# Performance work log

Measured on AMD Instinct MI355X. Metric: run time of the kernel, lower is better.

## Reference

```python
import jax, jax.numpy as jnp
import numpy as np

DIM = 768
HEADS = 12
HEAD_DIM = DIM // HEADS
HIDDEN = 4 * DIM
LS_INIT = 1e-5
EPS = 1e-5


def layernorm(x, g, b):
    mu = jnp.mean(x, axis=-1, keepdims=True)
    var = jnp.mean(jnp.square(x - mu), axis=-1, keepdims=True)
    return (x - mu) * jax.lax.rsqrt(var + EPS) * g + b


def setup_inputs() -> dict:
    key = jax.random.key(0)
    ks = jax.random.split(key, 8)
    s = lambda fan_in: 1.0 / np.sqrt(fan_in)
    return {
        "x": jax.random.normal(ks[0], (8, 1024, DIM), dtype=jnp.float32),
        "ln1_g": jnp.ones((DIM,), jnp.float32),
        "ln1_b": jnp.zeros((DIM,), jnp.float32),
        "w_qkv": jax.random.uniform(ks[1], (3 * DIM, DIM), jnp.float32, -s(DIM), s(DIM)),
        "w_proj": jax.random.uniform(ks[2], (DIM, DIM), jnp.float32, -s(DIM), s(DIM)),
        "b_proj": jnp.zeros((DIM,), jnp.float32),
        "ls1_g": jnp.full((DIM,), LS_INIT, jnp.float32),
        "ln2_g": jnp.ones((DIM,), jnp.float32),
        "ln2_b": jnp.zeros((DIM,), jnp.float32),
        "w_fc1": jax.random.uniform(ks[3], (HIDDEN, DIM), jnp.float32, -s(DIM), s(DIM)),
        "b_fc1": jnp.zeros((HIDDEN,), jnp.float32),
        "w_fc2": jax.random.uniform(ks[4], (DIM, HIDDEN), jnp.float32, -s(HIDDEN), s(HIDDEN)),
        "b_fc2": jnp.zeros((DIM,), jnp.float32),
        "ls2_g": jnp.full((DIM,), LS_INIT, jnp.float32),
    }


def reference(x, ln1_g, ln1_b, w_qkv, w_proj, b_proj, ls1_g,
              ln2_g, ln2_b, w_fc1, b_fc1, w_fc2, b_fc2, ls2_g):
    B, N, C = x.shape
    # --- attention branch ---
    h = layernorm(x, ln1_g, ln1_b)
    qkv = h @ w_qkv.T  # [B,N,3C]
    qkv = qkv.reshape(B, N, 3, HEADS, HEAD_DIM)
    q, k, v = qkv[:, :, 0], qkv[:, :, 1], qkv[:, :, 2]  # [B,N,H,D]
    scale = 1.0 / np.sqrt(HEAD_DIM)
    attn = jnp.einsum("bqhd,bkhd->bhqk", q, k) * scale
    attn = jax.nn.softmax(attn, axis=-1)
    o = jnp.einsum("bhqk,bkhd->bqhd", attn, v).reshape(B, N, C)
    o = o @ w_proj.T + b_proj
    x = x + ls1_g * o
    # --- MLP branch ---
    h = layernorm(x, ln2_g, ln2_b)
    h = jax.nn.gelu(h @ w_fc1.T + b_fc1, approximate=False)
    h = h @ w_fc2.T + b_fc2
    x = x + ls2_g * h
    return x
```

## Files before the change

### kernel.cpp

```cpp
#include <hip/hip_runtime.h>
#include <cstdint>
#include <cstddef>

typedef __bf16 bf16x8 __attribute__((ext_vector_type(8)));
typedef float f32x4 __attribute__((ext_vector_type(4)));
typedef int i32x4 __attribute__((ext_vector_type(4)));
typedef int i32x8 __attribute__((ext_vector_type(8)));

__device__ __forceinline__ void gload16(const void* g, void* l) {
  __builtin_amdgcn_global_load_lds((const __attribute__((address_space(1))) void*)g,
                                   (__attribute__((address_space(3))) void*)l, 16, 0, 0);
}

__device__ __forceinline__ float exp2_fast(float x) {
  float r;
  asm("v_exp_f32 %0, %1" : "=v"(r) : "v"(x));
  return r;
}
__device__ __forceinline__ float rcp_fast(float x) {
  float r;
  asm("v_rcp_f32 %0, %1" : "=v"(r) : "v"(x));
  return r;
}

__device__ __forceinline__ unsigned int f32_to_fp4(float x) {
  const float a = fabsf(x);
  unsigned int c = a < 0.25f ? 0u : a < 0.75f ? 1u : a < 1.25f ? 2u : a < 1.75f ? 3u
                 : a < 2.5f  ? 4u : a < 3.5f  ? 5u : a < 5.0f  ? 6u : 7u;
  return c | ((__float_as_uint(x) >> 28) & 8u);
}
__device__ __forceinline__ unsigned char pack_fp4x2(float lo, float hi) {
  return (unsigned char)(f32_to_fp4(lo) | (f32_to_fp4(hi) << 4));
}

template<int N> __device__ __forceinline__ void wait_vm() {
  if constexpr (N == 0)       asm volatile("s_waitcnt vmcnt(0)" ::: "memory");
  else if constexpr (N == 3)  asm volatile("s_waitcnt vmcnt(3)" ::: "memory");
  else if constexpr (N == 4)  asm volatile("s_waitcnt vmcnt(4)" ::: "memory");
}

#define S_BARRIER() __builtin_amdgcn_s_barrier()
#define WAIT_LGKM() asm volatile("s_waitcnt lgkmcnt(0)" ::: "memory")

__global__ __launch_bounds__(256) void ln_kernel(const float* __restrict__ x,
    const float* __restrict__ g, const float* __restrict__ b,
    unsigned char* __restrict__ out)
{
  __shared__ float red[8];
  const int row = blockIdx.x, t = threadIdx.x;
  const float* xr = x + (size_t)row * 768;
  float v0 = xr[t], v1 = xr[t + 256], v2 = xr[t + 512];
  float s = v0 + v1 + v2;
  float q = v0 * v0 + v1 * v1 + v2 * v2;
  #pragma unroll
  for (int off = 32; off > 0; off >>= 1) {
    s += __shfl_xor(s, off, 64);
    q += __shfl_xor(q, off, 64);
  }
  const int w = t >> 6;
  if ((t & 63) == 0) { red[w] = s; red[4 + w] = q; }
  __syncthreads();
  s = red[0] + red[1] + red[2] + red[3];
  q = red[4] + red[5] + red[6] + red[7];
  const float mu = s * (1.0f / 768.0f);
  const float var = q * (1.0f / 768.0f) - mu * mu;
  const float rstd = rsqrtf(var + 1e-5f);
  unsigned char* orow = out + (size_t)row * 384;
  for (int p = t; p < 384; p += 256) {
    const int c = 2 * p;
    const float y0 = (xr[c]     - mu) * rstd * g[c]     + b[c];
    const float y1 = (xr[c + 1] - mu) * rstd * g[c + 1] + b[c + 1];
    orow[p] = pack_fp4x2(y0, y1);
  }
}

__global__ __launch_bounds__(256) void cast4_kernel(
    const float* __restrict__ i0, const float* __restrict__ i1,
    const float* __restrict__ i2, const float* __restrict__ i3,
    unsigned char* __restrict__ o0, unsigned char* __restrict__ o1,
    unsigned char* __restrict__ o2, unsigned char* __restrict__ o3)
{
  const int n0 = 2304 * 768 / 4, n1 = 768 * 768 / 4;
  const int n2 = 3072 * 768 / 4, n3 = 768 * 3072 / 4;
  const int total = n0 + n1 + n2 + n3;
  for (int i = blockIdx.x * 256 + threadIdx.x; i < total; i += gridDim.x * 256) {
    const float* in; unsigned char* out; int j = i; float ws = 128.0f;
    if (j < n0) { in = i0; out = o0; }
    else if ((j -= n0) < n1) { in = i1; out = o1; }
    else if ((j -= n1) < n2) { in = i2; out = o2; }
    else { j -= n2; in = i3; out = o3; ws = 256.0f; }
    float4 v = ((const float4*)in)[j];
    const unsigned char b0 = pack_fp4x2(v.x * ws, v.y * ws);
    const unsigned char b1 = pack_fp4x2(v.z * ws, v.w * ws);
    ((unsigned short*)out)[j] = (unsigned short)(b0 | (b1 << 8));
  }
}

template<int MODE>
__global__ __launch_bounds__(256) void gemm_kernel(
    const unsigned char* __restrict__ A, const unsigned char* __restrict__ W, int K,
    unsigned int scaleB,
    const float* __restrict__ bias, const float* __restrict__ resid,
    const float* __restrict__ ls, float* __restrict__ outf,
    unsigned char* __restrict__ outb,
    __bf16* __restrict__ qo, __bf16* __restrict__ ko, __bf16* __restrict__ vo)
{
  constexpr int FM = 4, FN = 2;
  __shared__ unsigned char As[2 * 128 * 64];
  __shared__ unsigned char Bs[2 * 64 * 64];

  const int nx = gridDim.x;
  const int nwg = nx * gridDim.y;
  const int orig = blockIdx.x + nx * blockIdx.y;
  const int nid = (orig & 7) * (nwg >> 3) + (orig >> 3);
  const int bx = nid % nx, by = nid / nx;

  const int t = threadIdx.x;
  const int lane = t & 63;
  const int w = t >> 6;
  const int wm = w >> 1, wn = w & 1;
  const int m0 = by * 128, n0 = bx * 64;
  const int rl = lane & 15, gs = lane >> 4;
  const int Kb2 = K >> 1;

  f32x4 acc[FM][FN];
  #pragma unroll
  for (int i = 0; i < FM; ++i)
    #pragma unroll
    for (int j = 0; j < FN; ++j) acc[i][j] = { 0.f, 0.f, 0.f, 0.f };

  const unsigned char* Asrc[2];
  const unsigned char* Bsrc1;
  #pragma unroll
  for (int i = 0; i < 2; ++i) {
    const int g = i * 256 + t, row = g >> 2, gc = g & 3;
    Asrc[i] = A + (size_t)(m0 + row) * Kb2 + ((gc ^ (row & 3)) << 4);
  }
  {
    const int row = t >> 2, gc = t & 3;
    Bsrc1 = W + (size_t)(n0 + row) * Kb2 + ((gc ^ (row & 3)) << 4);
  }

  auto stage = [&](int kt, int buf) {
    const int k0 = kt << 6;
    #pragma unroll
    for (int i = 0; i < 2; ++i)
      gload16(Asrc[i] + k0, As + buf * 8192 + (i * 256 + t) * 16);
    gload16(Bsrc1 + k0, Bs + buf * 4096 + t * 16);
  };

  auto ld16 = [&](const unsigned char* rowbase, int sw) -> i32x8 {
    const i32x4 v = *(const i32x4*)(rowbase + ((gs ^ sw) << 4));
    i32x8 r;
    r[0] = v[0]; r[1] = v[1]; r[2] = v[2]; r[3] = v[3];
    r[4] = 0; r[5] = 0; r[6] = 0; r[7] = 0;
    return r;
  };

  const int nk = K >> 7;
  stage(0, 0);

  #pragma unroll 2
  for (int kt = 0; kt < nk; ++kt) {
    const int cur = kt & 1;
    if (kt + 1 < nk) { stage(kt + 1, cur ^ 1); wait_vm<3>(); }
    else             { wait_vm<0>(); }
    S_BARRIER();

    const unsigned char* Ac = As + cur * 8192;
    const unsigned char* Bc = Bs + cur * 4096;
    i32x8 af[FM], bfr[FN];
    #pragma unroll
    for (int fm = 0; fm < FM; ++fm) {
      const int row = wm * 64 + fm * 16 + rl;
      af[fm] = ld16(Ac + row * 64, row & 3);
    }
    #pragma unroll
    for (int fn = 0; fn < FN; ++fn) {
      const int row = wn * 32 + fn * 16 + rl;
      bfr[fn] = ld16(Bc + row * 64, row & 3);
    }
    #pragma unroll
    for (int fm = 0; fm < FM; ++fm)
      #pragma unroll
      for (int fn = 0; fn < FN; ++fn)
        acc[fm][fn] = __builtin_amdgcn_mfma_scale_f32_16x16x128_f8f6f4(
            af[fm], bfr[fn], acc[fm][fn],
            4, 4,
            0, 0x7F7F7F7F,
            0, (int)scaleB);

    S_BARRIER();
  }

  #pragma unroll
  for (int fm = 0; fm < FM; ++fm) {
    const int rbase = m0 + wm * 64 + fm * 16 + gs * 4;
    #pragma unroll
    for (int fn = 0; fn < FN; ++fn) {
      const int c = n0 + wn * 32 + fn * 16 + rl;
      #pragma unroll
      for (int b = 0; b < 4; ++b) {
        const int r = rbase + b;
        const float val = acc[fm][fn][b];
        if constexpr (MODE == 0) {
          const int sec = c / 768;
          const int cc = c - sec * 768;
          const int hh = cc >> 6, d = cc & 63;
          const int batch = r >> 10, n = r & 1023;
          const size_t bh = (size_t)(batch * 12 + hh);
          if (sec == 0)      qo[(bh * 1024 + n) * 64 + d] = (__bf16)(val * 0.1803368801111204f);
          else if (sec == 1) ko[(bh * 1024 + n) * 64 + d] = (__bf16)val;
          else               vo[(bh * 64 + d) * 1024 + n] = (__bf16)val;
        } else if constexpr (MODE == 1) {
          const size_t idx = (size_t)r * 768 + c;
          outf[idx] = resid[idx] + ls[c] * (val + bias[c]);
        } else if constexpr (MODE == 2) {
          const float h = val + bias[c];
          const float z = h * (1.0f + 0.044715f * h * h);
          const float e = exp2_fast(2.3021181f * z);
          const float gl = h - h * rcp_fast(1.0f + e);
          const float gp = __shfl_xor(gl, 1, 64);
          if ((lane & 1) == 0)
            outb[(size_t)r * 1536 + (c >> 1)] = pack_fp4x2(gl, gp);
        } else {
          const size_t idx = (size_t)r * 768 + c;
          outf[idx] = resid[idx] + ls[c] * (val + bias[c]);
        }
      }
    }
  }
}

__global__ __launch_bounds__(256, 3) void attn_kernel(
    const __bf16* __restrict__ Q, const __bf16* __restrict__ Kb,
    const __bf16* __restrict__ Vt, unsigned char* __restrict__ Ob)
{
  __shared__ __bf16 Ks[2][64 * 64];
  __shared__ __bf16 Vs[2][64 * 64];
  __shared__ __bf16 P_lds[4][32 * 72];

  const int nid = blockIdx.x;
  const int b7 = nid & 7, rest = nid >> 3;
  const int qt = rest & 7;
  const int bh = b7 + ((rest >> 3) << 3);

  const int t = threadIdx.x, lane = t & 63, w = t >> 6;
  const int rl = lane & 15, gs = lane >> 4;
  const int q0 = qt * 128 + w * 32;
  const __bf16* Qh = Q  + (size_t)bh * 1024 * 64;
  const char*   Kg = (const char*)(Kb + (size_t)bh * 1024 * 64);
  const char*   Vg = (const char*)(Vt + (size_t)bh * 64 * 1024);
  __bf16* Pw = &P_lds[w][0];

  const int g0 = w * 64 + lane;
  const int g1 = 256 + g0;
  const int r0 = g0 >> 3, sb0 = (g0 & 7) ^ (r0 & 7);
  const int r1 = g1 >> 3, sb1 = (g1 & 7) ^ (r1 & 7);

  bf16x8 aq[2][2];
  #pragma unroll
  for (int m = 0; m < 2; ++m)
    #pragma unroll
    for (int ks = 0; ks < 2; ++ks)
      aq[m][ks] = *(const bf16x8*)(Qh + (size_t)(q0 + m * 16 + rl) * 64 + ks * 32 + gs * 8);

  f32x4 accO[2][4];
  #pragma unroll
  for (int m = 0; m < 2; ++m)
    #pragma unroll
    for (int d = 0; d < 4; ++d) accO[m][d] = { 0.f, 0.f, 0.f, 0.f };
  float L[2][4];
  #pragma unroll
  for (int m = 0; m < 2; ++m)
    #pragma unroll
    for (int b = 0; b < 4; ++b) L[m][b] = 0.f;

  {
    gload16(Kg + (size_t)r0 * 128 + sb0 * 16, (char*)Ks[0] + g0 * 16);
    gload16(Kg + (size_t)r1 * 128 + sb1 * 16, (char*)Ks[0] + g1 * 16);
    gload16(Vg + (size_t)r0 * 2048 + sb0 * 16, (char*)Vs[0] + g0 * 16);
    gload16(Vg + (size_t)r1 * 2048 + sb1 * 16, (char*)Vs[0] + g1 * 16);
  }

  for (int tile = 0; tile < 16; ++tile) {
    const int cur = tile & 1;
    if (tile + 1 < 16) {
      const int nxt = cur ^ 1;
      const size_t kofs = (size_t)(tile + 1) * 64;
      gload16(Kg + (kofs + r0) * 128 + sb0 * 16, (char*)Ks[nxt] + g0 * 16);
      gload16(Kg + (kofs + r1) * 128 + sb1 * 16, (char*)Ks[nxt] + g1 * 16);
      gload16(Vg + (size_t)r0 * 2048 + kofs * 2 + sb0 * 16, (char*)Vs[nxt] + g0 * 16);
      gload16(Vg + (size_t)r1 * 2048 + kofs * 2 + sb1 * 16, (char*)Vs[nxt] + g1 * 16);
      wait_vm<4>();
    } else {
      wait_vm<0>();
    }
    S_BARRIER();

    const __bf16* Kc = Ks[cur];
    const __bf16* Vc = Vs[cur];

    f32x4 s[2][4];
    #pragma unroll
    for (int m = 0; m < 2; ++m)
      #pragma unroll
      for (int ct = 0; ct < 4; ++ct) s[m][ct] = { 0.f, 0.f, 0.f, 0.f };
    __builtin_amdgcn_s_setprio(1);
    #pragma unroll
    for (int ct = 0; ct < 4; ++ct) {
      #pragma unroll
      for (int ks = 0; ks < 2; ++ks) {
        const int row = ct * 16 + rl;
        const int blk = (ks * 4 + gs) ^ (row & 7);
        bf16x8 kf = *(const bf16x8*)(Kc + row * 64 + blk * 8);
        s[0][ct] = __builtin_amdgcn_mfma_f32_16x16x32_bf16(aq[0][ks], kf, s[0][ct], 0, 0, 0);
        s[1][ct] = __builtin_amdgcn_mfma_f32_16x16x32_bf16(aq[1][ks], kf, s[1][ct], 0, 0, 0);
      }
    }
    __builtin_amdgcn_s_setprio(0);

    #pragma unroll
    for (int m = 0; m < 2; ++m) {
      #pragma unroll
      for (int b = 0; b < 4; ++b) {
        float rs = 0.f;
        #pragma unroll
        for (int ct = 0; ct < 4; ++ct) {
          const float p = exp2_fast(s[m][ct][b]);
          rs += p;
          Pw[(m * 16 + gs * 4 + b) * 72 + ct * 16 + rl] = (__bf16)p;
        }
        L[m][b] += rs;
      }
    }

    WAIT_LGKM();
    bf16x8 ap[2][2];
    #pragma unroll
    for (int m = 0; m < 2; ++m)
      #pragma unroll
      for (int ks = 0; ks < 2; ++ks)
        ap[m][ks] = *(const bf16x8*)(Pw + (m * 16 + rl) * 72 + ks * 32 + gs * 8);

    __builtin_amdgcn_s_setprio(1);
    #pragma unroll
    for (int dt = 0; dt < 4; ++dt) {
      #pragma unroll
      for (int ks = 0; ks < 2; ++ks) {
        const int row = dt * 16 + rl;
        const int blk = (ks * 4 + gs) ^ (row & 7);
        bf16x8 vf = *(const bf16x8*)(Vc + row * 64 + blk * 8);
        accO[0][dt] = __builtin_amdgcn_mfma_f32_16x16x32_bf16(ap[0][ks], vf, accO[0][dt], 0, 0, 0);
        accO[1][dt] = __builtin_amdgcn_mfma_f32_16x16x32_bf16(ap[1][ks], vf, accO[1][dt], 0, 0, 0);
      }
    }
    __builtin_amdgcn_s_setprio(0);

    S_BARRIER();
  }

  float invL[2][4];
  #pragma unroll
  for (int m = 0; m < 2; ++m)
    #pragma unroll
    for (int b = 0; b < 4; ++b) {
      float rs = L[m][b];
      #pragma unroll
      for (int off = 1; off < 16; off <<= 1) rs += __shfl_xor(rs, off, 16);
      invL[m][b] = 1.0f / rs;
    }

  const int batch = bh / 12, hh = bh - batch * 12;
  #pragma unroll
  for (int m = 0; m < 2; ++m) {
    const size_t rowbase = (size_t)batch * 1024 + qt * 128 + w * 32 + m * 16 + gs * 4;
    #pragma unroll
    for (int dt = 0; dt < 4; ++dt)
      #pragma unroll
      for (int b = 0; b < 4; ++b) {
        const float val = accO[m][dt][b] * invL[m][b];
        const float vp = __shfl_xor(val, 1, 64);
        if ((lane & 1) == 0)
          Ob[(rowbase + b) * 384 + ((hh * 64 + dt * 16 + rl) >> 1)] = pack_fp4x2(val, vp);
      }
  }
}

extern "C" void kernel_launch(void* const* d_in, const int* in_sizes, int n_in,
                              void* d_out, int out_size, void* d_ws, size_t ws_size,
                              hipStream_t stream) {
  const float* x      = (const float*)d_in[0];
  const float* ln1_g  = (const float*)d_in[1];
  const float* ln1_b  = (const float*)d_in[2];
  const float* w_qkv  = (const float*)d_in[3];
  const float* w_proj = (const float*)d_in[4];
  const float* b_proj = (const float*)d_in[5];
  const float* ls1    = (const float*)d_in[6];
  const float* ln2_g  = (const float*)d_in[7];
  const float* ln2_b  = (const float*)d_in[8];
  const float* w_fc1  = (const float*)d_in[9];
  const float* b_fc1  = (const float*)d_in[10];
  const float* w_fc2  = (const float*)d_in[11];
  const float* b_fc2  = (const float*)d_in[12];
  const float* ls2    = (const float*)d_in[13];
  float* out = (float*)d_out;

  char* ws = (char*)d_ws;
  size_t off = 0;
  auto alloc = [&](size_t bytes) { char* p = ws + off; off += (bytes + 255) & ~(size_t)255; return p; };
  unsigned char* h1    = (unsigned char*)alloc(8192ull * 384);
  unsigned char* wqkv4 = (unsigned char*)alloc(2304ull * 384);
  unsigned char* wprj4 = (unsigned char*)alloc(768ull * 384);
  unsigned char* wfc14 = (unsigned char*)alloc(3072ull * 384);
  unsigned char* wfc24 = (unsigned char*)alloc(768ull * 1536);
  __bf16* Qb    = (__bf16*)alloc(8192ull * 768 * 2);
  __bf16* Kb    = (__bf16*)alloc(8192ull * 768 * 2);
  __bf16* Vt    = (__bf16*)alloc(8192ull * 768 * 2);
  float*  out1  = (float*)alloc(8192ull * 768 * 4);
  unsigned char* fc1o = (unsigned char*)alloc(8192ull * 1536);
  unsigned char* h2   = (unsigned char*)alloc(8192ull * 384);

  const unsigned int SC7 = 0x78787878u;
  const unsigned int SC8 = 0x77777777u;

  ln_kernel<<<8192, 256, 0, stream>>>(x, ln1_g, ln1_b, h1);
  cast4_kernel<<<2048, 256, 0, stream>>>(w_qkv, w_proj, w_fc1, w_fc2,
                                         wqkv4, wprj4, wfc14, wfc24);

  gemm_kernel<0><<<dim3(36, 64), 256, 0, stream>>>(h1, wqkv4, 768, SC7,
      nullptr, nullptr, nullptr, nullptr, nullptr, Qb, Kb, Vt);

  attn_kernel<<<96 * 8, 256, 0, stream>>>(Qb, Kb, Vt, h1);

  gemm_kernel<1><<<dim3(12, 64), 256, 0, stream>>>(h1, wprj4, 768, SC7,
      b_proj, x, ls1, out1, nullptr, nullptr, nullptr, nullptr);

  ln_kernel<<<8192, 256, 0, stream>>>(out1, ln2_g, ln2_b, h2);

  gemm_kernel<2><<<dim3(48, 64), 256, 0, stream>>>(h2, wfc14, 768, SC7,
      b_fc1, nullptr, nullptr, nullptr, fc1o, nullptr, nullptr, nullptr);

  gemm_kernel<3><<<dim3(12, 64), 256, 0, stream>>>(fc1o, wfc24, 3072, SC8,
      b_fc2, out1, ls2, out, nullptr, nullptr, nullptr, nullptr);
}
```

Baseline: 179.3 us.

## Switch activation operands from FP4 to FP8 in mixed-precision GEMMs

Activations (LayerNorm outputs, attention output, GELU output) are now quantized to FP8 e4m3 with the hardware convert instruction instead of the software FP4 packing. The GEMM A tile doubles to 128 bytes per row with 8-way swizzle, and the scaled MFMA runs with an FP8 A operand and an FP4 B operand. This removes the branchy FP4 conversion and shuffle-pair packing and likely improves accuracy, but doubles activation memory traffic and A-tile LDS use.

```diff
diff --git a/kernel.cpp b/kernel.cpp
--- a/kernel.cpp
+++ b/kernel.cpp
@@ -21,6 +21,11 @@
   float r;
   asm("v_rcp_f32 %0, %1" : "=v"(r) : "v"(x));
   return r;
+}
+
+__device__ __forceinline__ unsigned char f32_to_fp8(float x) {
+  int p = __builtin_amdgcn_cvt_pk_fp8_f32(x, 0.f, 0, false);
+  return (unsigned char)(p & 0xff);
 }
 
 __device__ __forceinline__ unsigned int f32_to_fp4(float x) {
@@ -35,8 +40,8 @@
 
 template<int N> __device__ __forceinline__ void wait_vm() {
   if constexpr (N == 0)       asm volatile("s_waitcnt vmcnt(0)" ::: "memory");
-  else if constexpr (N == 3)  asm volatile("s_waitcnt vmcnt(3)" ::: "memory");
   else if constexpr (N == 4)  asm volatile("s_waitcnt vmcnt(4)" ::: "memory");
+  else if constexpr (N == 5)  asm volatile("s_waitcnt vmcnt(5)" ::: "memory");
 }
 
 #define S_BARRIER() __builtin_amdgcn_s_barrier()
@@ -65,13 +70,10 @@
   const float mu = s * (1.0f / 768.0f);
   const float var = q * (1.0f / 768.0f) - mu * mu;
   const float rstd = rsqrtf(var + 1e-5f);
-  unsigned char* orow = out + (size_t)row * 384;
-  for (int p = t; p < 384; p += 256) {
-    const int c = 2 * p;
-    const float y0 = (xr[c]     - mu) * rstd * g[c]     + b[c];
-    const float y1 = (xr[c + 1] - mu) * rstd * g[c + 1] + b[c + 1];
-    orow[p] = pack_fp4x2(y0, y1);
-  }
+  unsigned char* orow = out + (size_t)row * 768;
+  orow[t]       = f32_to_fp8((v0 - mu) * rstd * g[t]       + b[t]);
+  orow[t + 256] = f32_to_fp8((v1 - mu) * rstd * g[t + 256] + b[t + 256]);
+  orow[t + 512] = f32_to_fp8((v2 - mu) * rstd * g[t + 512] + b[t + 512]);
 }
 
 __global__ __launch_bounds__(256) void cast4_kernel(
@@ -106,7 +108,7 @@
     __bf16* __restrict__ qo, __bf16* __restrict__ ko, __bf16* __restrict__ vo)
 {
   constexpr int FM = 4, FN = 2;
-  __shared__ unsigned char As[2 * 128 * 64];
+  __shared__ unsigned char As[2 * 128 * 128];
   __shared__ unsigned char Bs[2 * 64 * 64];
 
   const int nx = gridDim.x;
@@ -129,27 +131,36 @@
     #pragma unroll
     for (int j = 0; j < FN; ++j) acc[i][j] = { 0.f, 0.f, 0.f, 0.f };
 
-  const unsigned char* Asrc[2];
+  const unsigned char* Asrc[4];
+  #pragma unroll
+  for (int i = 0; i < 4; ++i) {
+    const int g = i * 256 + t, row = g >> 3, gc = g & 7;
+    Asrc[i] = A + (size_t)(m0 + row) * K + ((gc ^ (row & 7)) << 4);
+  }
   const unsigned char* Bsrc1;
-  #pragma unroll
-  for (int i = 0; i < 2; ++i) {
-    const int g = i * 256 + t, row = g >> 2, gc = g & 3;
-    Asrc[i] = A + (size_t)(m0 + row) * Kb2 + ((gc ^ (row & 3)) << 4);
-  }
   {
     const int row = t >> 2, gc = t & 3;
     Bsrc1 = W + (size_t)(n0 + row) * Kb2 + ((gc ^ (row & 3)) << 4);
   }
 
   auto stage = [&](int kt, int buf) {
-    const int k0 = kt << 6;
-    #pragma unroll
-    for (int i = 0; i < 2; ++i)
-      gload16(Asrc[i] + k0, As + buf * 8192 + (i * 256 + t) * 16);
-    gload16(Bsrc1 + k0, Bs + buf * 4096 + t * 16);
+    const int ka = kt << 7;
+    const int kb = kt << 6;
+    #pragma unroll
+    for (int i = 0; i < 4; ++i)
+      gload16(Asrc[i] + ka, As + buf * 16384 + (i * 256 + t) * 16);
+    gload16(Bsrc1 + kb, Bs + buf * 4096 + t * 16);
   };
 
-  auto ld16 = [&](const unsigned char* rowbase, int sw) -> i32x8 {
+  auto ldA = [&](const unsigned char* rowbase, int sw) -> i32x8 {
+    const i32x4 lo = *(const i32x4*)(rowbase + (((2 * gs + 0) ^ sw) << 4));
+    const i32x4 hi = *(const i32x4*)(rowbase + (((2 * gs + 1) ^ sw) << 4));
+    i32x8 r;
+    r[0] = lo[0]; r[1] = lo[1]; r[2] = lo[2]; r[3] = lo[3];
+    r[4] = hi[0]; r[5] = hi[1]; r[6] = hi[2]; r[7] = hi[3];
+    return r;
+  };
+  auto ldB = [&](const unsigned char* rowbase, int sw) -> i32x8 {
     const i32x4 v = *(const i32x4*)(rowbase + ((gs ^ sw) << 4));
     i32x8 r;
     r[0] = v[0]; r[1] = v[1]; r[2] = v[2]; r[3] = v[3];
@@ -163,22 +174,22 @@
   #pragma unroll 2
   for (int kt = 0; kt < nk; ++kt) {
     const int cur = kt & 1;
-    if (kt + 1 < nk) { stage(kt + 1, cur ^ 1); wait_vm<3>(); }
+    if (kt + 1 < nk) { stage(kt + 1, cur ^ 1); wait_vm<5>(); }
     else             { wait_vm<0>(); }
     S_BARRIER();
 
-    const unsigned char* Ac = As + cur * 8192;
+    const unsigned char* Ac = As + cur * 16384;
     const unsigned char* Bc = Bs + cur * 4096;
     i32x8 af[FM], bfr[FN];
     #pragma unroll
     for (int fm = 0; fm < FM; ++fm) {
       const int row = wm * 64 + fm * 16 + rl;
-      af[fm] = ld16(Ac + row * 64, row & 3);
+      af[fm] = ldA(Ac + row * 128, row & 7);
     }
     #pragma unroll
     for (int fn = 0; fn < FN; ++fn) {
       const int row = wn * 32 + fn * 16 + rl;
-      bfr[fn] = ld16(Bc + row * 64, row & 3);
+      bfr[fn] = ldB(Bc + row * 64, row & 3);
     }
     #pragma unroll
     for (int fm = 0; fm < FM; ++fm)
@@ -186,7 +197,7 @@
       for (int fn = 0; fn < FN; ++fn)
         acc[fm][fn] = __builtin_amdgcn_mfma_scale_f32_16x16x128_f8f6f4(
             af[fm], bfr[fn], acc[fm][fn],
-            4, 4,
+            0, 4,
             0, 0x7F7F7F7F,
             0, (int)scaleB);
 
@@ -220,9 +231,7 @@
           const float z = h * (1.0f + 0.044715f * h * h);
           const float e = exp2_fast(2.3021181f * z);
           const float gl = h - h * rcp_fast(1.0f + e);
-          const float gp = __shfl_xor(gl, 1, 64);
-          if ((lane & 1) == 0)
-            outb[(size_t)r * 1536 + (c >> 1)] = pack_fp4x2(gl, gp);
+          outb[(size_t)r * 3072 + c] = f32_to_fp8(gl);
         } else {
           const size_t idx = (size_t)r * 768 + c;
           outf[idx] = resid[idx] + ls[c] * (val + bias[c]);
@@ -378,12 +387,8 @@
     #pragma unroll
     for (int dt = 0; dt < 4; ++dt)
       #pragma unroll
-      for (int b = 0; b < 4; ++b) {
-        const float val = accO[m][dt][b] * invL[m][b];
-        const float vp = __shfl_xor(val, 1, 64);
-        if ((lane & 1) == 0)
-          Ob[(rowbase + b) * 384 + ((hh * 64 + dt * 16 + rl) >> 1)] = pack_fp4x2(val, vp);
-      }
+      for (int b = 0; b < 4; ++b)
+        Ob[(rowbase + b) * 768 + hh * 64 + dt * 16 + rl] = f32_to_fp8(accO[m][dt][b] * invL[m][b]);
   }
 }
 
@@ -409,7 +414,7 @@
   char* ws = (char*)d_ws;
   size_t off = 0;
   auto alloc = [&](size_t bytes) { char* p = ws + off; off += (bytes + 255) & ~(size_t)255; return p; };
-  unsigned char* h1    = (unsigned char*)alloc(8192ull * 384);
+  unsigned char* h1    = (unsigned char*)alloc(8192ull * 768);
   unsigned char* wqkv4 = (unsigned char*)alloc(2304ull * 384);
   unsigned char* wprj4 = (unsigned char*)alloc(768ull * 384);
   unsigned char* wfc14 = (unsigned char*)alloc(3072ull * 384);
@@ -418,8 +423,8 @@
   __bf16* Kb    = (__bf16*)alloc(8192ull * 768 * 2);
   __bf16* Vt    = (__bf16*)alloc(8192ull * 768 * 2);
   float*  out1  = (float*)alloc(8192ull * 768 * 4);
-  unsigned char* fc1o = (unsigned char*)alloc(8192ull * 1536);
-  unsigned char* h2   = (unsigned char*)alloc(8192ull * 384);
+  unsigned char* fc1o = (unsigned char*)alloc(8192ull * 3072);
+  unsigned char* h2   = (unsigned char*)alloc(8192ull * 768);
 
   const unsigned int SC7 = 0x78787878u;
   const unsigned int SC8 = 0x77777777u;
```

Result: no change. 175.8 us, median of 3 (-2.0%).
